# Kernel optimization log

Hardware: AMD Instinct MI355X
Metric: run time of the kernel (lower is better)

## Reference

```python
import jax, jax.numpy as jnp
import numpy as np

N_HEAD, N_KV, HEAD_DIM, GATE_CH = 16, 4, 128, 32

def _rope(x, cos, sin):
    d = x.shape[3] // 2
    x1, x2 = x[..., :d], x[..., d:]
    return jnp.concatenate([x1 * cos + x2 * sin, x1 * (-sin) + x2 * cos], axis=3)

def _rmsnorm(x):
    xf = x.astype(jnp.float32)
    return (x * jax.lax.rsqrt(jnp.mean(xf * xf, axis=-1, keepdims=True) + 1e-6)).astype(x.dtype)

def setup_inputs() -> dict:
    key = jax.random.key(0)
    ks = jax.random.split(key, 9)
    B, T, C = 2, 2048, 2048
    return {
        "x":  jax.random.normal(ks[0], (B, T, C), jnp.float32),
        "ve": jax.random.normal(ks[1], (B, T, N_KV * HEAD_DIM), jnp.float32),
        "cos": jax.random.uniform(ks[2], (T, 1, HEAD_DIM // 2), jnp.float32),
        "sin": jax.random.uniform(ks[3], (T, 1, HEAD_DIM // 2), jnp.float32),
        "Wq": jax.random.normal(ks[4], (C, N_HEAD * HEAD_DIM), jnp.float32) * 0.02,
        "Wk": jax.random.normal(ks[5], (C, N_KV * HEAD_DIM), jnp.float32) * 0.02,
        "Wv": jax.random.normal(ks[6], (C, N_KV * HEAD_DIM), jnp.float32) * 0.02,
        "Wg": jax.random.normal(ks[7], (GATE_CH, N_KV), jnp.float32) * 0.02,
        "Wo": jax.random.normal(ks[8], (C, C), jnp.float32) * 0.02,
        "window": 1024,
    }

def reference(x, ve, cos, sin, Wq, Wk, Wv, Wg, Wo, window):
    B, T, C = x.shape
    q = (x @ Wq).reshape(B, T, N_HEAD, HEAD_DIM)
    k = (x @ Wk).reshape(B, T, N_KV, HEAD_DIM)
    v = (x @ Wv).reshape(B, T, N_KV, HEAD_DIM)
    # value-embedding gate (ve_gate active for this layer)
    gate = 2.0 * jax.nn.sigmoid(x[..., :GATE_CH] @ Wg)  # (B,T,N_KV)
    v = v + gate[..., None] * ve.reshape(B, T, N_KV, HEAD_DIM)
    q, k = _rope(q, cos, sin), _rope(k, cos, sin)
    q, k = _rmsnorm(q), _rmsnorm(k)
    # GQA: repeat kv heads (repeat_interleave over head dim)
    groups = N_HEAD // N_KV
    k = jnp.repeat(k, groups, axis=2)
    v = jnp.repeat(v, groups, axis=2)
    scale = 1.0 / np.sqrt(HEAD_DIM)
    scores = jnp.einsum("bthd,bshd->bhts", q, k) * scale  # (B,H,T,T)
    idx = jnp.arange(T)
    diff = idx[None, :] - idx[:, None]  # diff[i,j] = j - i, as in torch code
    mask = (diff >= 0) & (diff < window)
    scores = jnp.where(mask[None, None], scores, -jnp.inf)
    p = jax.nn.softmax(scores, axis=-1)
    y = jnp.einsum("bhts,bshd->bthd", p, v).reshape(B, T, C)
    return y @ Wo
```

## Files before the change

### kernel.cpp

```cpp
#include <hip/hip_runtime.h>
#include <hip/hip_bf16.h>
#include <cstdint>

typedef __hip_bfloat16 bf16;
typedef __attribute__((ext_vector_type(8))) short short8;
typedef __attribute__((ext_vector_type(4))) short short4v;
typedef __attribute__((ext_vector_type(4))) float f32x4;

#define T_   2048
#define CDIM 2048
#define NH   16
#define NKV  4
#define HD   128
#define QSCALE (0.08838834764831845f * 1.44269504088896340f)

__device__ __forceinline__ void gload_lds16(const void* g, void* l) {
  __builtin_amdgcn_global_load_lds(
      (const __attribute__((address_space(1))) void*)g,
      (__attribute__((address_space(3))) void*)l, 16, 0, 0);
}

template <int G> __device__ __forceinline__ void vm_gate() {
  if constexpr (G == 6)      asm volatile("s_waitcnt vmcnt(6)" ::: "memory");
  else if constexpr (G == 5) asm volatile("s_waitcnt vmcnt(5)" ::: "memory");
  else                       asm volatile("s_waitcnt vmcnt(0)" ::: "memory");
}

__global__ __launch_bounds__(256) void cast_x_kernel(const float4* __restrict__ in,
                                                     ushort4* __restrict__ out, int n4) {
  int i = blockIdx.x * 256 + threadIdx.x;
  if (i >= n4) return;
  float4 v = in[i];
  union { bf16 h[4]; ushort4 u; } cv;
  cv.h[0] = __float2bfloat16(v.x);
  cv.h[1] = __float2bfloat16(v.y);
  cv.h[2] = __float2bfloat16(v.z);
  cv.h[3] = __float2bfloat16(v.w);
  out[i] = cv.u;
}

__global__ __launch_bounds__(256) void cast_transpose(const float* __restrict__ W,
                                                      bf16* __restrict__ WT,
                                                      int K, int N) {
  __shared__ float tile[32][33];
  int k0 = blockIdx.y * 32, n0 = blockIdx.x * 32;
  int r = threadIdx.x >> 5, c = threadIdx.x & 31;
  for (int i = 0; i < 4; ++i)
    tile[r + i * 8][c] = W[(size_t)(k0 + r + i * 8) * N + n0 + c];
  __syncthreads();
  for (int i = 0; i < 4; ++i)
    WT[(size_t)(n0 + r + i * 8) * K + k0 + c] = __float2bfloat16(tile[c][r + i * 8]);
}

template <int MREP, int NREP, typename CT>
__global__ __launch_bounds__(512, 2) void gemm_pp(const bf16* __restrict__ A,
                                                  const bf16* __restrict__ BT,
                                                  CT* __restrict__ C,
                                                  int N, int K, int RY, int RX) {
  constexpr int BM = MREP * 32;
  constexpr int BN = NREP * 64;
  constexpr int QN = (MREP == 8) ? 4 : 2;
  constexpr int MI = MREP / 4;
  constexpr int GATE = NREP + QN - 1;
  __shared__ __align__(16) bf16 sA[2][BM * 64];
  __shared__ __align__(16) bf16 sB[2][BN * 64];

  int tid = threadIdx.x;
  int lane = tid & 63, w = tid >> 6;
  int wm = w >> 2, wn = w & 3;
  int lr = lane & 15, lk = lane >> 4;

  int xcd = blockIdx.x & 7, t = blockIdx.x >> 3;
  int by = (xcd >> 1) * RY + t / RX;
  int bx = (xcd & 1) * RX + t % RX;
  int m0 = by * BM, n0 = bx * BN;

  f32x4 acc[MREP][NREP];
#pragma unroll
  for (int m = 0; m < MREP; ++m)
#pragma unroll
    for (int n = 0; n < NREP; ++n) acc[m][n] = (f32x4){0.f, 0.f, 0.f, 0.f};

  const bf16* Abase = A + (size_t)m0 * K;
  const bf16* Bbase = BT + (size_t)n0 * K;

  auto stageB = [&](int p, int kt) {
    int kb = kt << 6;
#pragma unroll
    for (int i = 0; i < NREP; ++i) {
      int c = i * 512 + tid;
      int r = c >> 3, sl = c & 7;
      gload_lds16(Bbase + (size_t)r * K + kb + ((sl ^ (r & 7)) << 3),
                  (char*)(&sB[p][0]) + c * 16);
    }
  };
  auto stageAq = [&](int p, int kt, int q) {
    int kb = kt << 6;
    int rbase = 32 * q + ((w & 3) << 3) + ((w >> 2) * (BM / 2));
    int r = rbase + (lane >> 3), sl = lane & 7;
    gload_lds16(Abase + (size_t)r * K + kb + ((sl ^ (r & 7)) << 3),
                (char*)(&sA[p][0]) + rbase * 128 + lane * 16);
  };

  int nk = K >> 6;
  stageB(0, 0);
#pragma unroll
  for (int q = 0; q < QN; ++q) stageAq(0, 0, q);
  stageB(1, 1);
#pragma unroll
  for (int q = 0; q < QN - 1; ++q) stageAq(1, 1, q);
  vm_gate<GATE>();
  __builtin_amdgcn_s_barrier();

#define READ_A_FRAGS(PH)                                                   \
  {                                                                        \
    _Pragma("unroll")                                                      \
    for (int mi = 0; mi < MI; ++mi) {                                      \
      int row = wm * (MREP * 16) + ((PH) * MI + mi) * 16 + lr;             \
      const char* rb = sAb + row * 128;                                    \
      int rx = (row & 7) << 4;                                             \
      af[mi][0] = *(const short8*)(rb + ((lk * 16) ^ rx));                 \
      af[mi][1] = *(const short8*)(rb + ((64 + lk * 16) ^ rx));            \
    }                                                                      \
  }
#define MFMA_PH(PH)                                                        \
  __builtin_amdgcn_s_setprio(1);                                           \
  _Pragma("unroll")                                                        \
  for (int kk = 0; kk < 2; ++kk)                                           \
    _Pragma("unroll")                                                      \
    for (int mi = 0; mi < MI; ++mi)                                        \
      _Pragma("unroll")                                                    \
      for (int n = 0; n < NREP; ++n)                                       \
        acc[(PH) * MI + mi][n] = __builtin_amdgcn_mfma_f32_16x16x32_bf16(  \
            af[mi][kk], bfr[n][kk], acc[(PH) * MI + mi][n], 0, 0, 0);      \
  __builtin_amdgcn_s_setprio(0);
#define LGKM_FENCE                                                         \
  asm volatile("s_waitcnt lgkmcnt(0)" ::: "memory");                       \
  __builtin_amdgcn_sched_barrier(0);

  for (int kt = 0; kt < nk; ++kt) {
    int p = kt & 1;
    const char* sAb = (const char*)(&sA[p][0]);
    const char* sBb = (const char*)(&sB[p][0]);
    short8 bfr[NREP][2], af[MI][2];

#pragma unroll
    for (int n = 0; n < NREP; ++n) {
      int row = wn * (NREP * 16) + n * 16 + lr;
      const char* rb = sBb + row * 128;
      int rx = (row & 7) << 4;
      bfr[n][0] = *(const short8*)(rb + ((lk * 16) ^ rx));
      bfr[n][1] = *(const short8*)(rb + ((64 + lk * 16) ^ rx));
    }
    READ_A_FRAGS(0);
    if (kt + 1 < nk) stageAq(p ^ 1, kt + 1, QN - 1);
    LGKM_FENCE;
    MFMA_PH(0);
    __builtin_amdgcn_s_barrier();

    READ_A_FRAGS(1);
    if (kt + 2 < nk) {
      stageB(p, kt + 2);
      if constexpr (QN == 4) stageAq(p, kt + 2, 0);
    }
    LGKM_FENCE;
    MFMA_PH(1);
    __builtin_amdgcn_s_barrier();

    READ_A_FRAGS(2);
    if (kt + 2 < nk) stageAq(p, kt + 2, (QN == 4) ? 1 : 0);
    LGKM_FENCE;
    MFMA_PH(2);
    __builtin_amdgcn_s_barrier();

    READ_A_FRAGS(3);
    if constexpr (QN == 4) {
      if (kt + 2 < nk) stageAq(p, kt + 2, 2);
    }
    LGKM_FENCE;
    MFMA_PH(3);
    if (kt + 2 < nk) vm_gate<GATE>();
    else             vm_gate<0>();
    __builtin_amdgcn_s_barrier();
  }
#undef READ_A_FRAGS
#undef MFMA_PH
#undef LGKM_FENCE

#pragma unroll
  for (int m = 0; m < MREP; ++m)
#pragma unroll
    for (int n = 0; n < NREP; ++n)
#pragma unroll
      for (int jj = 0; jj < 4; ++jj) {
        size_t idx = (size_t)(m0 + wm * (MREP * 16) + m * 16 + lk * 4 + jj) * N +
                     n0 + wn * (NREP * 16) + n * 16 + lr;
        if constexpr (__is_same(CT, float))
          C[idx] = acc[m][n][jj];
        else
          C[idx] = __float2bfloat16(acc[m][n][jj]);
      }
}

__global__ __launch_bounds__(256) void epilogue_kernel(
    const bf16* __restrict__ qkv, const float* __restrict__ x,
    const float* __restrict__ ve, const float* __restrict__ cosT,
    const float* __restrict__ sinT, const float* __restrict__ Wg,
    bf16* __restrict__ qn, bf16* __restrict__ kn, bf16* __restrict__ vT) {
  int row = blockIdx.x;
  int bi = row >> 11, t = row & 2047;
  int tid = threadIdx.x, lane = tid & 63, w = tid >> 6;
  __shared__ float gate[NKV];
  size_t rb = (size_t)row * 3072;

  if (tid < 128) {
    int g = tid >> 5, i = tid & 31;
    float p = x[(size_t)row * CDIM + i] * Wg[i * 4 + g];
    p += __shfl_xor(p, 1);  p += __shfl_xor(p, 2);
    p += __shfl_xor(p, 4);  p += __shfl_xor(p, 8);
    p += __shfl_xor(p, 16);
    if (i == 0) gate[g] = 2.f / (1.f + __expf(-p));
  }
  __syncthreads();

  float cv = cosT[t * 64 + lane];
  float sv = sinT[t * 64 + lane];

  for (int it = 0; it < 4; ++it) {
    int h = it * 4 + w;
    float x1 = __bfloat162float(qkv[rb + h * 128 + lane]);
    float x2 = __bfloat162float(qkv[rb + h * 128 + 64 + lane]);
    float y1 = x1 * cv + x2 * sv;
    float y2 = x2 * cv - x1 * sv;
    float ss = y1 * y1 + y2 * y2;
    ss += __shfl_xor(ss, 1);  ss += __shfl_xor(ss, 2);  ss += __shfl_xor(ss, 4);
    ss += __shfl_xor(ss, 8);  ss += __shfl_xor(ss, 16); ss += __shfl_xor(ss, 32);
    float r = rsqrtf(ss * (1.f / 128.f) + 1e-6f) * QSCALE;
    size_t ob = (size_t)row * (NH * HD) + h * 128;
    qn[ob + lane] = __float2bfloat16(y1 * r);
    qn[ob + 64 + lane] = __float2bfloat16(y2 * r);
  }
  {
    int h = w;
    float x1 = __bfloat162float(qkv[rb + 2048 + h * 128 + lane]);
    float x2 = __bfloat162float(qkv[rb + 2048 + h * 128 + 64 + lane]);
    float y1 = x1 * cv + x2 * sv;
    float y2 = x2 * cv - x1 * sv;
    float ss = y1 * y1 + y2 * y2;
    ss += __shfl_xor(ss, 1);  ss += __shfl_xor(ss, 2);  ss += __shfl_xor(ss, 4);
    ss += __shfl_xor(ss, 8);  ss += __shfl_xor(ss, 16); ss += __shfl_xor(ss, 32);
    float r = rsqrtf(ss * (1.f / 128.f) + 1e-6f);
    size_t ob = (size_t)row * (NKV * HD) + h * 128;
    kn[ob + lane] = __float2bfloat16(y1 * r);
    kn[ob + 64 + lane] = __float2bfloat16(y2 * r);
  }
  for (int e = tid; e < 512; e += 256) {
    int kv = e >> 7, d = e & 127;
    float val = __bfloat162float(qkv[rb + 2560 + e]) + gate[kv] * ve[(size_t)row * 512 + e];
    vT[((size_t)(bi * NKV + kv) * HD + d) * T_ + t] = __float2bfloat16(val);
  }
}

__global__ __launch_bounds__(256, 3) void attn_kernel(
    const bf16* __restrict__ qn, const bf16* __restrict__ kn,
    const bf16* __restrict__ vT, bf16* __restrict__ y,
    const int* __restrict__ winp) {
  __shared__ __align__(16) bf16 sK[64 * 128];
  __shared__ __align__(16) bf16 sV[128 * 64];

  int win = *winp;
  int id = blockIdx.x;
  int g  = id & 7;
  int bi = g >> 2, kvh = g & 3;
  int rem = id >> 3;
  int h  = kvh * 4 + (rem & 3);
  int jslot = (rem >> 2) & 7;
  int s5 = rem >> 5;
  int q0i = (s5 == 0) ? (2 * jslot) : (s5 == 1) ? (2 * jslot + 1)
          : (s5 == 2) ? (16 + jslot) : (31 - jslot);
  int q0 = q0i << 6;
  int tid = threadIdx.x;
  int lane = tid & 63, w = tid >> 6;
  int lr = lane & 15, lk = lane >> 4;

  short8 qf[4];
  {
    const bf16* qrow = qn + (size_t)(bi * T_ + q0 + w * 16 + lr) * (NH * HD) + h * HD;
#pragma unroll
    for (int c = 0; c < 4; ++c) qf[c] = *(const short8*)(qrow + c * 32 + lk * 8);
  }

  int kge[4], klb[4], vge[4], vlbA[4], vlbB[4];
#pragma unroll
  for (int i = 0; i < 4; ++i) {
    int c = i * 256 + tid;
    int kr = c >> 4, ks = c & 15;
    kge[i] = kr * (NKV * HD) + ks * 8;
    klb[i] = kr * 256 + ((ks ^ (kr & 7)) << 4);
    int vr = c >> 3, vs = c & 7;
    vge[i] = vr * T_ + vs * 8;
    int hh = vs >> 2, m = vs & 3, a = m >> 1;
    int sA = 8 * ((2 * m) & 3) + 4 * a;
    int sB = 8 * ((2 * m + 1) & 3) + 4 * a;
    int tA = 64 * hh + 2 * sA, tB = 64 * hh + 2 * sB;
    vlbA[i] = vr * 128 + (((tA >> 4) ^ (vr & 7)) << 4) + (tA & 15);
    vlbB[i] = vr * 128 + (((tB >> 4) ^ (vr & 7)) << 4) + (tB & 15);
  }
  const bf16* kpane = kn + (size_t)bi * T_ * (NKV * HD) + kvh * HD;
  const bf16* vpane = vT + (size_t)(bi * NKV + kvh) * HD * T_;

  short8 kreg[4], vreg[4];
  auto LOAD = [&](int jtx) {
    const bf16* kb = kpane + (size_t)(jtx << 6) * (NKV * HD);
    const bf16* vb = vpane + (jtx << 6);
#pragma unroll
    for (int i = 0; i < 4; ++i) kreg[i] = *(const short8*)(kb + kge[i]);
#pragma unroll
    for (int i = 0; i < 4; ++i) vreg[i] = *(const short8*)(vb + vge[i]);
  };
  auto WRITE = [&]() {
#pragma unroll
    for (int i = 0; i < 4; ++i) *(short8*)((char*)sK + klb[i]) = kreg[i];
#pragma unroll
    for (int i = 0; i < 4; ++i) {
      union { short8 s8; short4v s4[2]; } u;
      u.s8 = vreg[i];
      *(short4v*)((char*)sV + vlbA[i]) = u.s4[0];
      *(short4v*)((char*)sV + vlbB[i]) = u.s4[1];
    }
  };

  f32x4 o[8];
#pragma unroll
  for (int i = 0; i < 8; ++i) o[i] = (f32x4){0.f, 0.f, 0.f, 0.f};
  float lpart = 0.f;

  int jt0 = q0 >> 6;
  int hi = q0 + 62 + win; if (hi > T_ - 1) hi = T_ - 1;
  int jt1 = hi >> 6;

  LOAD(jt0);
  WRITE();
  if (jt0 < jt1) LOAD(jt0 + 1);
  asm volatile("s_waitcnt lgkmcnt(0)\n\ts_barrier" ::: "memory");

  int irow = q0 + w * 16 + lr;
  int klo = lk * 4;

  for (int jt = jt0; jt <= jt1; ++jt) {
    int j0 = jt << 6;

    f32x4 s[4];
#pragma unroll
    for (int sub = 0; sub < 4; ++sub) s[sub] = (f32x4){0.f, 0.f, 0.f, 0.f};
    __builtin_amdgcn_s_setprio(1);
#pragma unroll
    for (int sub = 0; sub < 4; ++sub) {
      int kr = sub * 16 + lr;
      int rx = (kr & 7) << 4;
      const char* rowb = (const char*)sK + kr * 256;
#pragma unroll
      for (int c = 0; c < 4; ++c) {
        short8 kf = *(const short8*)(rowb + ((c * 64 + lk * 16) ^ rx));
        s[sub] = __builtin_amdgcn_mfma_f32_16x16x32_bf16(kf, qf[c], s[sub], 0, 0, 0);
      }
    }
    __builtin_amdgcn_s_setprio(0);

    bool full = (j0 >= q0 + 64) && (j0 + 64 <= q0 + win);
    int koff = j0 - irow;

    unsigned pk[8];
#pragma unroll
    for (int sub = 0; sub < 4; ++sub) {
      float p0 = exp2f(s[sub][0]), p1 = exp2f(s[sub][1]);
      float p2 = exp2f(s[sub][2]), p3 = exp2f(s[sub][3]);
      if (!full) {
        int base = koff + sub * 16 + klo;
        p0 = ((unsigned)(base + 0) < (unsigned)win) ? p0 : 0.f;
        p1 = ((unsigned)(base + 1) < (unsigned)win) ? p1 : 0.f;
        p2 = ((unsigned)(base + 2) < (unsigned)win) ? p2 : 0.f;
        p3 = ((unsigned)(base + 3) < (unsigned)win) ? p3 : 0.f;
      }
      lpart += (p0 + p1) + (p2 + p3);
      asm("v_cvt_pk_bf16_f32 %0, %1, %2" : "=v"(pk[sub * 2])     : "v"(p0), "v"(p1));
      asm("v_cvt_pk_bf16_f32 %0, %1, %2" : "=v"(pk[sub * 2 + 1]) : "v"(p2), "v"(p3));
    }
    union { unsigned u[4]; short8 s8; } c0, c1;
    c0.u[0] = pk[0]; c0.u[1] = pk[1]; c0.u[2] = pk[2]; c0.u[3] = pk[3];
    c1.u[0] = pk[4]; c1.u[1] = pk[5]; c1.u[2] = pk[6]; c1.u[3] = pk[7];
    short8 pf0 = c0.s8, pf1 = c1.s8;

    __builtin_amdgcn_s_setprio(1);
#pragma unroll
    for (int nb = 0; nb < 8; ++nb) {
      int vr = nb * 16 + lr;
      int vrx = (vr & 7) << 4;
      const char* vb = (const char*)sV + vr * 128;
      short8 vf0 = *(const short8*)(vb + ((lk * 16) ^ vrx));
      short8 vf1 = *(const short8*)(vb + ((64 + lk * 16) ^ vrx));
      o[nb] = __builtin_amdgcn_mfma_f32_16x16x32_bf16(pf0, vf0, o[nb], 0, 0, 0);
      o[nb] = __builtin_amdgcn_mfma_f32_16x16x32_bf16(pf1, vf1, o[nb], 0, 0, 0);
    }
    __builtin_amdgcn_s_setprio(0);

    asm volatile("s_waitcnt lgkmcnt(0)\n\ts_barrier" ::: "memory");
    if (jt < jt1) {
      WRITE();
      if (jt + 1 < jt1) LOAD(jt + 2);
      asm volatile("s_waitcnt lgkmcnt(0)\n\ts_barrier" ::: "memory");
    }
  }

  float l = lpart;
  l += __shfl_xor(l, 16);
  l += __shfl_xor(l, 32);
#pragma unroll
  for (int jj = 0; jj < 4; ++jj) {
    float inv = 1.f / __shfl(l, klo + jj);
    size_t ob = (size_t)(bi * T_ + q0 + w * 16 + klo + jj) * (NH * HD) + h * HD;
#pragma unroll
    for (int nb = 0; nb < 8; ++nb)
      y[ob + nb * 16 + lr] = __float2bfloat16(o[nb][jj] * inv);
  }
}

extern "C" void kernel_launch(void* const* d_in, const int* in_sizes, int n_in,
                              void* d_out, int out_size, void* d_ws, size_t ws_size,
                              hipStream_t stream) {
  const float* x    = (const float*)d_in[0];
  const float* ve   = (const float*)d_in[1];
  const float* cosT = (const float*)d_in[2];
  const float* sinT = (const float*)d_in[3];
  const float* Wq   = (const float*)d_in[4];
  const float* Wk   = (const float*)d_in[5];
  const float* Wv   = (const float*)d_in[6];
  const float* Wg   = (const float*)d_in[7];
  const float* Wo   = (const float*)d_in[8];
  const int*   win  = (const int*)d_in[9];
  float* out = (float*)d_out;

  char* ws = (char*)d_ws;
  bf16*  xb   = (bf16*)(ws);
  bf16*  wT   = (bf16*)(ws + 16777216);
  bf16*  woT  = (bf16*)(ws + 29360128);
  bf16*  qkvb = (bf16*)(ws + 37748736);
  bf16*  qn   = (bf16*)(ws + 62914560);
  bf16*  kn   = (bf16*)(ws + 79691776);
  bf16*  vTb  = (bf16*)(ws + 83886080);
  bf16*  y    = qkvb;

  cast_x_kernel<<<8192, 256, 0, stream>>>((const float4*)x, (ushort4*)xb, 2097152);
  cast_transpose<<<dim3(64, 64), 256, 0, stream>>>(Wq, wT, 2048, 2048);
  cast_transpose<<<dim3(16, 64), 256, 0, stream>>>(Wk, wT + (size_t)2048 * 2048, 2048, 512);
  cast_transpose<<<dim3(16, 64), 256, 0, stream>>>(Wv, wT + (size_t)2560 * 2048, 2048, 512);
  cast_transpose<<<dim3(64, 64), 256, 0, stream>>>(Wo, woT, 2048, 2048);

  gemm_pp<8, 3, bf16><<<256, 512, 0, stream>>>(xb, wT, qkvb, 3072, 2048, 4, 8);
  epilogue_kernel<<<4096, 256, 0, stream>>>(qkvb, x, ve, cosT, sinT, Wg, qn, kn, vTb);
  attn_kernel<<<1024, 256, 0, stream>>>(qn, kn, vTb, y, win);
  gemm_pp<4, 4, float><<<256, 512, 0, stream>>>(y, woT, out, 2048, 2048, 8, 4);
}
```

Measured before the change: 198.1 us.

## Double query rows per attention block and add pre-MFMA barriers in GEMM

The attention kernel now processes 128 query rows per block (32 per wave, as two 16-row fragments). Each K/V tile loaded into LDS is therefore reused by twice as many queries, and the grid is halved to 512 blocks with launch bounds lowered to 2 blocks per CU. The load-balancing query-slot permutation is replaced by a linear mapping. The GEMM pipeline also gains an extra workgroup barrier before each MFMA phase, which lines waves up but adds sync cost. The attention change raises register pressure and processes more fully masked tiles per block, and the linear mapping may cause tail imbalance.

```diff
diff --git a/kernel.cpp b/kernel.cpp
--- a/kernel.cpp
+++ b/kernel.cpp
@@ -134,7 +134,7 @@
         acc[(PH) * MI + mi][n] = __builtin_amdgcn_mfma_f32_16x16x32_bf16(  \
             af[mi][kk], bfr[n][kk], acc[(PH) * MI + mi][n], 0, 0, 0);      \
   __builtin_amdgcn_s_setprio(0);
-#define LGKM_FENCE                                                         \
+#define WAIT_LGKM                                                          \
   asm volatile("s_waitcnt lgkmcnt(0)" ::: "memory");                       \
   __builtin_amdgcn_sched_barrier(0);
 
@@ -154,7 +154,8 @@
     }
     READ_A_FRAGS(0);
     if (kt + 1 < nk) stageAq(p ^ 1, kt + 1, QN - 1);
-    LGKM_FENCE;
+    __builtin_amdgcn_s_barrier();
+    WAIT_LGKM;
     MFMA_PH(0);
     __builtin_amdgcn_s_barrier();
 
@@ -163,13 +164,15 @@
       stageB(p, kt + 2);
       if constexpr (QN == 4) stageAq(p, kt + 2, 0);
     }
-    LGKM_FENCE;
+    __builtin_amdgcn_s_barrier();
+    WAIT_LGKM;
     MFMA_PH(1);
     __builtin_amdgcn_s_barrier();
 
     READ_A_FRAGS(2);
     if (kt + 2 < nk) stageAq(p, kt + 2, (QN == 4) ? 1 : 0);
-    LGKM_FENCE;
+    __builtin_amdgcn_s_barrier();
+    WAIT_LGKM;
     MFMA_PH(2);
     __builtin_amdgcn_s_barrier();
 
@@ -177,7 +180,8 @@
     if constexpr (QN == 4) {
       if (kt + 2 < nk) stageAq(p, kt + 2, 2);
     }
-    LGKM_FENCE;
+    __builtin_amdgcn_s_barrier();
+    WAIT_LGKM;
     MFMA_PH(3);
     if (kt + 2 < nk) vm_gate<GATE>();
     else             vm_gate<0>();
@@ -185,7 +189,7 @@
   }
 #undef READ_A_FRAGS
 #undef MFMA_PH
-#undef LGKM_FENCE
+#undef WAIT_LGKM
 
 #pragma unroll
   for (int m = 0; m < MREP; ++m)
@@ -261,7 +265,7 @@
   }
 }
 
-__global__ __launch_bounds__(256, 3) void attn_kernel(
+__global__ __launch_bounds__(256, 2) void attn_kernel(
     const bf16* __restrict__ qn, const bf16* __restrict__ kn,
     const bf16* __restrict__ vT, bf16* __restrict__ y,
     const int* __restrict__ winp) {
@@ -274,20 +278,20 @@
   int bi = g >> 2, kvh = g & 3;
   int rem = id >> 3;
   int h  = kvh * 4 + (rem & 3);
-  int jslot = (rem >> 2) & 7;
-  int s5 = rem >> 5;
-  int q0i = (s5 == 0) ? (2 * jslot) : (s5 == 1) ? (2 * jslot + 1)
-          : (s5 == 2) ? (16 + jslot) : (31 - jslot);
-  int q0 = q0i << 6;
+  int q0 = (rem >> 2) << 7;
   int tid = threadIdx.x;
   int lane = tid & 63, w = tid >> 6;
   int lr = lane & 15, lk = lane >> 4;
 
-  short8 qf[4];
+  short8 qfA[4], qfB[4];
   {
-    const bf16* qrow = qn + (size_t)(bi * T_ + q0 + w * 16 + lr) * (NH * HD) + h * HD;
-#pragma unroll
-    for (int c = 0; c < 4; ++c) qf[c] = *(const short8*)(qrow + c * 32 + lk * 8);
+    const bf16* qrA = qn + (size_t)(bi * T_ + q0 + w * 32 + lr) * (NH * HD) + h * HD;
+    const bf16* qrB = qrA + (size_t)16 * (NH * HD);
+#pragma unroll
+    for (int c = 0; c < 4; ++c) {
+      qfA[c] = *(const short8*)(qrA + c * 32 + lk * 8);
+      qfB[c] = *(const short8*)(qrB + c * 32 + lk * 8);
+    }
   }
 
   int kge[4], klb[4], vge[4], vlbA[4], vlbB[4];
@@ -330,13 +334,16 @@
     }
   };
 
-  f32x4 o[8];
-#pragma unroll
-  for (int i = 0; i < 8; ++i) o[i] = (f32x4){0.f, 0.f, 0.f, 0.f};
-  float lpart = 0.f;
+  f32x4 o0[8], o1[8];
+#pragma unroll
+  for (int i = 0; i < 8; ++i) {
+    o0[i] = (f32x4){0.f, 0.f, 0.f, 0.f};
+    o1[i] = (f32x4){0.f, 0.f, 0.f, 0.f};
+  }
+  float lp0 = 0.f, lp1 = 0.f;
 
   int jt0 = q0 >> 6;
-  int hi = q0 + 62 + win; if (hi > T_ - 1) hi = T_ - 1;
+  int hi = q0 + 126 + win; if (hi > T_ - 1) hi = T_ - 1;
   int jt1 = hi >> 6;
 
   LOAD(jt0);
@@ -344,15 +351,18 @@
   if (jt0 < jt1) LOAD(jt0 + 1);
   asm volatile("s_waitcnt lgkmcnt(0)\n\ts_barrier" ::: "memory");
 
-  int irow = q0 + w * 16 + lr;
+  int irow0 = q0 + w * 32 + lr;
   int klo = lk * 4;
 
   for (int jt = jt0; jt <= jt1; ++jt) {
     int j0 = jt << 6;
 
-    f32x4 s[4];
-#pragma unroll
-    for (int sub = 0; sub < 4; ++sub) s[sub] = (f32x4){0.f, 0.f, 0.f, 0.f};
+    f32x4 s0[4], s1[4];
+#pragma unroll
+    for (int sub = 0; sub < 4; ++sub) {
+      s0[sub] = (f32x4){0.f, 0.f, 0.f, 0.f};
+      s1[sub] = (f32x4){0.f, 0.f, 0.f, 0.f};
+    }
     __builtin_amdgcn_s_setprio(1);
 #pragma unroll
     for (int sub = 0; sub < 4; ++sub) {
@@ -362,34 +372,61 @@
 #pragma unroll
       for (int c = 0; c < 4; ++c) {
         short8 kf = *(const short8*)(rowb + ((c * 64 + lk * 16) ^ rx));
-        s[sub] = __builtin_amdgcn_mfma_f32_16x16x32_bf16(kf, qf[c], s[sub], 0, 0, 0);
+        s0[sub] = __builtin_amdgcn_mfma_f32_16x16x32_bf16(kf, qfA[c], s0[sub], 0, 0, 0);
+        s1[sub] = __builtin_amdgcn_mfma_f32_16x16x32_bf16(kf, qfB[c], s1[sub], 0, 0, 0);
       }
     }
     __builtin_amdgcn_s_setprio(0);
 
-    bool full = (j0 >= q0 + 64) && (j0 + 64 <= q0 + win);
-    int koff = j0 - irow;
-
-    unsigned pk[8];
-#pragma unroll
-    for (int sub = 0; sub < 4; ++sub) {
-      float p0 = exp2f(s[sub][0]), p1 = exp2f(s[sub][1]);
-      float p2 = exp2f(s[sub][2]), p3 = exp2f(s[sub][3]);
-      if (!full) {
-        int base = koff + sub * 16 + klo;
-        p0 = ((unsigned)(base + 0) < (unsigned)win) ? p0 : 0.f;
-        p1 = ((unsigned)(base + 1) < (unsigned)win) ? p1 : 0.f;
-        p2 = ((unsigned)(base + 2) < (unsigned)win) ? p2 : 0.f;
-        p3 = ((unsigned)(base + 3) < (unsigned)win) ? p3 : 0.f;
+    bool full = (j0 >= q0 + 128) && (j0 + 64 <= q0 + win);
+    int koff0 = j0 - irow0;
+    int koff1 = koff0 - 16;
+
+    short8 pA0, pA1, pB0, pB1;
+    {
+      unsigned pk[8];
+#pragma unroll
+      for (int sub = 0; sub < 4; ++sub) {
+        float p0 = exp2f(s0[sub][0]), p1 = exp2f(s0[sub][1]);
+        float p2 = exp2f(s0[sub][2]), p3 = exp2f(s0[sub][3]);
+        if (!full) {
+          int base = koff0 + sub * 16 + klo;
+          p0 = ((unsigned)(base + 0) < (unsigned)win) ? p0 : 0.f;
+          p1 = ((unsigned)(base + 1) < (unsigned)win) ? p1 : 0.f;
+          p2 = ((unsigned)(base + 2) < (unsigned)win) ? p2 : 0.f;
+          p3 = ((unsigned)(base + 3) < (unsigned)win) ? p3 : 0.f;
+        }
+        lp0 += (p0 + p1) + (p2 + p3);
+        asm("v_cvt_pk_bf16_f32 %0, %1, %2" : "=v"(pk[sub * 2])     : "v"(p0), "v"(p1));
+        asm("v_cvt_pk_bf16_f32 %0, %1, %2" : "=v"(pk[sub * 2 + 1]) : "v"(p2), "v"(p3));
       }
-      lpart += (p0 + p1) + (p2 + p3);
-      asm("v_cvt_pk_bf16_f32 %0, %1, %2" : "=v"(pk[sub * 2])     : "v"(p0), "v"(p1));
-      asm("v_cvt_pk_bf16_f32 %0, %1, %2" : "=v"(pk[sub * 2 + 1]) : "v"(p2), "v"(p3));
-    }
-    union { unsigned u[4]; short8 s8; } c0, c1;
-    c0.u[0] = pk[0]; c0.u[1] = pk[1]; c0.u[2] = pk[2]; c0.u[3] = pk[3];
-    c1.u[0] = pk[4]; c1.u[1] = pk[5]; c1.u[2] = pk[6]; c1.u[3] = pk[7];
-    short8 pf0 = c0.s8, pf1 = c1.s8;
+      union { unsigned u[4]; short8 s8; } c0, c1;
+      c0.u[0] = pk[0]; c0.u[1] = pk[1]; c0.u[2] = pk[2]; c0.u[3] = pk[3];
+      c1.u[0] = pk[4]; c1.u[1] = pk[5]; c1.u[2] = pk[6]; c1.u[3] = pk[7];
+      pA0 = c0.s8; pA1 = c1.s8;
+    }
+    {
+      unsigned pk[8];
+#pragma unroll
+      for (int sub = 0; sub < 4; ++sub) {
+        float p0 = exp2f(s1[sub][0]), p1 = exp2f(s1[sub][1]);
+        float p2 = exp2f(s1[sub][2]), p3 = exp2f(s1[sub][3]);
+        if (!full) {
+          int base = koff1 + sub * 16 + klo;
+          p0 = ((unsigned)(base + 0) < (unsigned)win) ? p0 : 0.f;
+          p1 = ((unsigned)(base + 1) < (unsigned)win) ? p1 : 0.f;
+          p2 = ((unsigned)(base + 2) < (unsigned)win) ? p2 : 0.f;
+          p3 = ((unsigned)(base + 3) < (unsigned)win) ? p3 : 0.f;
+        }
+        lp1 += (p0 + p1) + (p2 + p3);
+        asm("v_cvt_pk_bf16_f32 %0, %1, %2" : "=v"(pk[sub * 2])     : "v"(p0), "v"(p1));
+        asm("v_cvt_pk_bf16_f32 %0, %1, %2" : "=v"(pk[sub * 2 + 1]) : "v"(p2), "v"(p3));
+      }
+      union { unsigned u[4]; short8 s8; } c0, c1;
+      c0.u[0] = pk[0]; c0.u[1] = pk[1]; c0.u[2] = pk[2]; c0.u[3] = pk[3];
+      c1.u[0] = pk[4]; c1.u[1] = pk[5]; c1.u[2] = pk[6]; c1.u[3] = pk[7];
+      pB0 = c0.s8; pB1 = c1.s8;
+    }
 
     __builtin_amdgcn_s_setprio(1);
 #pragma unroll
@@ -399,8 +436,10 @@
       const char* vb = (const char*)sV + vr * 128;
       short8 vf0 = *(const short8*)(vb + ((lk * 16) ^ vrx));
       short8 vf1 = *(const short8*)(vb + ((64 + lk * 16) ^ vrx));
-      o[nb] = __builtin_amdgcn_mfma_f32_16x16x32_bf16(pf0, vf0, o[nb], 0, 0, 0);
-      o[nb] = __builtin_amdgcn_mfma_f32_16x16x32_bf16(pf1, vf1, o[nb], 0, 0, 0);
+      o0[nb] = __builtin_amdgcn_mfma_f32_16x16x32_bf16(pA0, vf0, o0[nb], 0, 0, 0);
+      o0[nb] = __builtin_amdgcn_mfma_f32_16x16x32_bf16(pA1, vf1, o0[nb], 0, 0, 0);
+      o1[nb] = __builtin_amdgcn_mfma_f32_16x16x32_bf16(pB0, vf0, o1[nb], 0, 0, 0);
+      o1[nb] = __builtin_amdgcn_mfma_f32_16x16x32_bf16(pB1, vf1, o1[nb], 0, 0, 0);
     }
     __builtin_amdgcn_s_setprio(0);
 
@@ -412,16 +451,20 @@
     }
   }
 
-  float l = lpart;
-  l += __shfl_xor(l, 16);
-  l += __shfl_xor(l, 32);
+  float l0 = lp0, l1 = lp1;
+  l0 += __shfl_xor(l0, 16); l0 += __shfl_xor(l0, 32);
+  l1 += __shfl_xor(l1, 16); l1 += __shfl_xor(l1, 32);
 #pragma unroll
   for (int jj = 0; jj < 4; ++jj) {
-    float inv = 1.f / __shfl(l, klo + jj);
-    size_t ob = (size_t)(bi * T_ + q0 + w * 16 + klo + jj) * (NH * HD) + h * HD;
-#pragma unroll
-    for (int nb = 0; nb < 8; ++nb)
-      y[ob + nb * 16 + lr] = __float2bfloat16(o[nb][jj] * inv);
+    float inv0 = 1.f / __shfl(l0, klo + jj);
+    float inv1 = 1.f / __shfl(l1, klo + jj);
+    size_t ob0 = (size_t)(bi * T_ + q0 + w * 32 + klo + jj) * (NH * HD) + h * HD;
+    size_t ob1 = ob0 + (size_t)16 * (NH * HD);
+#pragma unroll
+    for (int nb = 0; nb < 8; ++nb) {
+      y[ob0 + nb * 16 + lr] = __float2bfloat16(o0[nb][jj] * inv0);
+      y[ob1 + nb * 16 + lr] = __float2bfloat16(o1[nb][jj] * inv1);
+    }
   }
 }
 
@@ -458,6 +501,6 @@
 
   gemm_pp<8, 3, bf16><<<256, 512, 0, stream>>>(xb, wT, qkvb, 3072, 2048, 4, 8);
   epilogue_kernel<<<4096, 256, 0, stream>>>(qkvb, x, ve, cosT, sinT, Wg, qn, kn, vTb);
-  attn_kernel<<<1024, 256, 0, stream>>>(qn, kn, vTb, y, win);
+  attn_kernel<<<512, 256, 0, stream>>>(qn, kn, vTb, y, win);
   gemm_pp<4, 4, float><<<256, 512, 0, stream>>>(y, woT, out, 2048, 2048, 8, 4);
 }
```

After: 195.6 us. No clear change (-1.3%).
